# Kernel optimization log

Hardware: AMD Instinct MI355X
Metric: run time of the kernel (lower is better)

Reference implementation:

```python
import jax, jax.numpy as jnp
import numpy as np

N_NODES = 50000
N_EDGES = 800000
F_NODE = 128
F_EDGE = 32
H = 64


def _gat_layer(x, row, col, e_emb, W, le_W, att_src, att_dst, att_edge, bias):
    """PyG GATConv (heads=1, concat=True) with edge_dim, incl. self loops.
    x: [N, Fin]; row/col: [E] int (src, dst); e_emb: [E, H].
    """
    N = x.shape[0]
    loop = jnp.arange(N, dtype=row.dtype)
    row_a = jnp.concatenate([row, loop])
    col_a = jnp.concatenate([col, loop])
    # self-loop edge attr = mean of edge embeddings (PyG fill_value='mean')
    e_mean = jnp.mean(e_emb, axis=0)
    e_all = jnp.concatenate([e_emb, jnp.broadcast_to(e_mean, (N, e_emb.shape[1]))], axis=0)

    h = x @ W.T                      # [N, H]
    a_src = h @ att_src              # [N]
    a_dst = h @ att_dst              # [N]
    a_edge = (e_all @ le_W.T) @ att_edge  # [E+N]

    alpha = jax.nn.leaky_relu(a_src[row_a] + a_dst[col_a] + a_edge, negative_slope=0.2)
    # segment softmax over destination node neighborhoods
    m = jax.ops.segment_max(alpha, col_a, num_segments=N)
    ex = jnp.exp(alpha - m[col_a])
    denom = jax.ops.segment_sum(ex, col_a, num_segments=N)
    w = ex / denom[col_a]            # [E+N]
    out = jax.ops.segment_sum(h[row_a] * w[:, None], col_a, num_segments=N)
    return out + bias


def setup_inputs() -> dict:
    key = jax.random.key(0)
    ks = jax.random.split(key, 20)
    s = 0.1
    inp = {
        "x": jax.random.normal(ks[0], (N_NODES, F_NODE), dtype=jnp.float32),
        "edge_attr": jax.random.normal(ks[1], (N_EDGES, F_EDGE), dtype=jnp.float32),
        "edge_index": jax.random.randint(ks[2], (2, N_EDGES), 0, N_NODES, dtype=jnp.int32),
        # edge encoder (Linear with bias)
        "enc_W": jax.random.normal(ks[3], (H, F_EDGE), dtype=jnp.float32) * s,
        "enc_b": jnp.zeros((H,), dtype=jnp.float32),
        # conv1 params
        "W1": jax.random.normal(ks[4], (H, F_NODE), dtype=jnp.float32) * s,
        "le1_W": jax.random.normal(ks[5], (H, H), dtype=jnp.float32) * s,
        "as1": jax.random.normal(ks[6], (H,), dtype=jnp.float32) * s,
        "ad1": jax.random.normal(ks[7], (H,), dtype=jnp.float32) * s,
        "ae1": jax.random.normal(ks[8], (H,), dtype=jnp.float32) * s,
        "b1": jnp.zeros((H,), dtype=jnp.float32),
        # conv2 params
        "W2": jax.random.normal(ks[9], (H, H), dtype=jnp.float32) * s,
        "le2_W": jax.random.normal(ks[10], (H, H), dtype=jnp.float32) * s,
        "as2": jax.random.normal(ks[11], (H,), dtype=jnp.float32) * s,
        "ad2": jax.random.normal(ks[12], (H,), dtype=jnp.float32) * s,
        "ae2": jax.random.normal(ks[13], (H,), dtype=jnp.float32) * s,
        "b2": jnp.zeros((H,), dtype=jnp.float32),
        # edge scorer MLP: Linear(2H, H) -> ReLU -> Linear(H, 1)
        "s1_W": jax.random.normal(ks[14], (H, 2 * H), dtype=jnp.float32) * s,
        "s1_b": jnp.zeros((H,), dtype=jnp.float32),
        "s2_W": jax.random.normal(ks[15], (1, H), dtype=jnp.float32) * s,
        "s2_b": jnp.zeros((1,), dtype=jnp.float32),
    }
    return inp


def reference(x, edge_attr, edge_index, enc_W, enc_b,
              W1, le1_W, as1, ad1, ae1, b1,
              W2, le2_W, as2, ad2, ae2, b2,
              s1_W, s1_b, s2_W, s2_b):
    row, col = edge_index[0], edge_index[1]
    edge_emb = edge_attr @ enc_W.T + enc_b           # [E, H]
    h = jax.nn.relu(_gat_layer(x, row, col, edge_emb, W1, le1_W, as1, ad1, ae1, b1))
    # dropout p=0.5 is identity in eval mode
    h = _gat_layer(h, row, col, edge_emb, W2, le2_W, as2, ad2, ae2, b2)
    ef = jnp.concatenate([h[row], h[col]], axis=1)   # [E, 2H]
    z = jax.nn.relu(ef @ s1_W.T + s1_b) @ s2_W.T + s2_b  # [E, 1]
    return jax.nn.sigmoid(z).squeeze(-1)             # [E]
```

## Files before the change

kernel.cpp:

```cpp
#include <hip/hip_runtime.h>
#include <cstdint>
#include <cstddef>

#define NN 50000
#define NE 800000
#define FN 128
#define FE 32
#define HD 64
#define SCAN_NB ((NN + 255) / 256)
#define EP_NB (NE / 256)
#define GM_NB ((NN + 63) / 64)

__device__ __forceinline__ float lrelu(float x) { return x > 0.f ? x : 0.2f * x; }

__device__ __forceinline__ unsigned omap(float f) {
  unsigned u = __float_as_uint(f);
  return (u & 0x80000000u) ? ~u : (u | 0x80000000u);
}
__device__ __forceinline__ float odec(unsigned u) {
  return __uint_as_float((u & 0x80000000u) ? (u ^ 0x80000000u) : ~u);
}

__global__ void k_small0(const float* __restrict__ le1W, const float* __restrict__ ae1,
                         const float* __restrict__ le2W, const float* __restrict__ ae2,
                         const float* __restrict__ encW, const float* __restrict__ encb,
                         const float* __restrict__ s1W,
                         float* __restrict__ small, float* __restrict__ Scomb) {
  __shared__ float sv1[64], sv2[64];
  int t = threadIdx.x;
  float v1 = 0.f, v2 = 0.f;
  for (int j = 0; j < 64; ++j) {
    v1 += le1W[j * 64 + t] * ae1[j];
    v2 += le2W[j * 64 + t] * ae2[j];
  }
  sv1[t] = v1; sv2[t] = v2;
  small[t] = v1; small[64 + t] = v2;
  float cb1 = encb[t] * v1, cb2 = encb[t] * v2;
  #pragma unroll
  for (int m = 32; m; m >>= 1) { cb1 += __shfl_xor(cb1, m); cb2 += __shfl_xor(cb2, m); }
  __syncthreads();
  if (t < 32) {
    float p1 = 0.f, p2 = 0.f;
    for (int i = 0; i < 64; ++i) {
      p1 += encW[i * 32 + t] * sv1[i];
      p2 += encW[i * 32 + t] * sv2[i];
    }
    small[128 + t] = p1; small[160 + t] = p2;
  }
  if (t == 0) { small[192] = cb1; small[193] = cb2; }
  for (int j = 0; j < 64; ++j) {
    Scomb[j * 64 + t] = s1W[j * 128 + t];
    Scomb[(64 + j) * 64 + t] = s1W[j * 128 + 64 + t];
  }
}

__global__ __launch_bounds__(256) void k_scanA(const int* __restrict__ counts,
                                               int* __restrict__ loc, int* __restrict__ blocksums) {
  int tid = threadIdx.x;
  int i = blockIdx.x * 256 + tid;
  int v = (i < NN) ? counts[i] : 0;
  int lane = tid & 63, wid = tid >> 6;
  int x = v;
  #pragma unroll
  for (int d = 1; d < 64; d <<= 1) {
    int y = __shfl_up(x, d);
    if (lane >= d) x += y;
  }
  __shared__ int ws[4], wpref[4];
  if (lane == 63) ws[wid] = x;
  __syncthreads();
  if (tid == 0) {
    int run = 0;
    #pragma unroll
    for (int w = 0; w < 4; ++w) { wpref[w] = run; run += ws[w]; }
    blocksums[blockIdx.x] = run;
  }
  __syncthreads();
  if (i < NN) loc[i] = x - v + wpref[wid];
}

__global__ __launch_bounds__(256) void k_scanB(int* __restrict__ blocksums, int* __restrict__ offa,
                                               float* __restrict__ small) {
  int tid = threadIdx.x;
  int v = (tid < SCAN_NB) ? blocksums[tid] : 0;
  int lane = tid & 63, wid = tid >> 6;
  int x = v;
  #pragma unroll
  for (int d = 1; d < 64; d <<= 1) {
    int y = __shfl_up(x, d);
    if (lane >= d) x += y;
  }
  __shared__ int ws[4], wpref[4];
  if (lane == 63) ws[wid] = x;
  __syncthreads();
  if (tid == 0) {
    int run = 0;
    #pragma unroll
    for (int w = 0; w < 4; ++w) { wpref[w] = run; run += ws[w]; }
    offa[NN] = run;
    small[194] = small[228] * (1.0f / NE);
    small[195] = small[229] * (1.0f / NE);
  }
  __syncthreads();
  if (tid < SCAN_NB) blocksums[tid] = x - v + wpref[wid];
}

__global__ __launch_bounds__(256) void k_scanC(int* __restrict__ offa, const int* __restrict__ blocksums) {
  int i = blockIdx.x * 256 + threadIdx.x;
  if (i < NN) offa[i] = offa[i] + blocksums[blockIdx.x];
}

__global__ __launch_bounds__(256) void k_fused0(const float* __restrict__ attr,
                                                const int* __restrict__ col,
                                                const float* __restrict__ small,
                                                float* __restrict__ a_e1, float* __restrict__ a_e2,
                                                int* __restrict__ rank,
                                                int* __restrict__ counts,
                                                float* __restrict__ sums,
                                                unsigned* __restrict__ maxi,
                                                const float* __restrict__ x, const float* __restrict__ W1,
                                                float* __restrict__ h1,
                                                const float* __restrict__ as, const float* __restrict__ ad,
                                                float* __restrict__ asrc, float* __restrict__ adst) {
  __shared__ float smem[8704];
  int tid = threadIdx.x;
  if (blockIdx.x < EP_NB) {
    float* sattr = smem;
    float* redbuf = smem + 8448;
    float sp1[32], sp2[32];
    #pragma unroll
    for (int j = 0; j < 8; ++j) {
      float4 v1 = ((const float4*)(small + 128))[j];
      float4 v2 = ((const float4*)(small + 160))[j];
      sp1[j*4+0] = v1.x; sp1[j*4+1] = v1.y; sp1[j*4+2] = v1.z; sp1[j*4+3] = v1.w;
      sp2[j*4+0] = v2.x; sp2[j*4+1] = v2.y; sp2[j*4+2] = v2.z; sp2[j*4+3] = v2.w;
    }
    float c1 = small[192], c2 = small[193];
    int e = blockIdx.x * 256 + tid;
    int c = col[e];
    const float4* ain = (const float4*)(attr + (size_t)blockIdx.x * 256 * FE);
    #pragma unroll
    for (int it = 0; it < 8; ++it) {
      int idx = it * 256 + tid;
      float4 v = ain[idx];
      int r = idx >> 3, ch = idx & 7;
      float* dst = &sattr[r * 33 + ch * 4];
      dst[0] = v.x; dst[1] = v.y; dst[2] = v.z; dst[3] = v.w;
    }
    __syncthreads();
    const float* myrow = &sattr[tid * 33];
    float d1 = c1, d2 = c2;
    #pragma unroll
    for (int j = 0; j < 32; ++j) {
      float a = myrow[j];
      d1 += a * sp1[j];
      d2 += a * sp2[j];
    }
    a_e1[e] = d1;
    a_e2[e] = d2;
    rank[e] = atomicAdd(&counts[c], 1);
    float s1 = d1, s2 = d2, m1 = d1, m2 = d2;
    #pragma unroll
    for (int m = 32; m; m >>= 1) {
      s1 += __shfl_xor(s1, m); s2 += __shfl_xor(s2, m);
      m1 = fmaxf(m1, __shfl_xor(m1, m)); m2 = fmaxf(m2, __shfl_xor(m2, m));
    }
    int wid = tid >> 6;
    if ((tid & 63) == 0) { redbuf[wid] = s1; redbuf[4 + wid] = s2; redbuf[8 + wid] = m1; redbuf[12 + wid] = m2; }
    __syncthreads();
    if (tid == 0) atomicAdd(&sums[0], redbuf[0] + redbuf[1] + redbuf[2] + redbuf[3]);
    if (tid == 1) atomicAdd(&sums[1], redbuf[4] + redbuf[5] + redbuf[6] + redbuf[7]);
    if (tid == 2) atomicMax(&maxi[2], omap(fmaxf(fmaxf(redbuf[8], redbuf[9]), fmaxf(redbuf[10], redbuf[11]))));
    if (tid == 3) atomicMax(&maxi[3], omap(fmaxf(fmaxf(redbuf[12], redbuf[13]), fmaxf(redbuf[14], redbuf[15]))));
  } else {
    float (*At)[68] = (float(*)[68])smem;
    float (*Bt)[68] = (float(*)[68])(smem + 4352);
    int m0 = (blockIdx.x - EP_NB) * 64;
    float acc[4][4] = {};
    for (int kc = 0; kc < 128; kc += 64) {
      #pragma unroll
      for (int it = 0; it < 4; ++it) {
        int idx = it * 256 + tid;
        int m = idx & 63, kv = idx >> 6;
        float4 bv = ((const float4*)(W1 + (size_t)m * 128 + kc))[kv];
        Bt[kv*4+0][m] = bv.x; Bt[kv*4+1][m] = bv.y; Bt[kv*4+2][m] = bv.z; Bt[kv*4+3][m] = bv.w;
        int gm = m0 + m;
        float4 av = make_float4(0.f, 0.f, 0.f, 0.f);
        if (gm < NN) av = ((const float4*)(x + (size_t)gm * 128 + kc))[kv];
        At[kv*4+0][m] = av.x; At[kv*4+1][m] = av.y; At[kv*4+2][m] = av.z; At[kv*4+3][m] = av.w;
      }
      __syncthreads();
      int tn = tid & 15, tm = tid >> 4;
      #pragma unroll 8
      for (int k = 0; k < 64; ++k) {
        float4 a4 = *(const float4*)&At[k][tm * 4];
        float4 b4 = *(const float4*)&Bt[k][tn * 4];
        acc[0][0] += a4.x*b4.x; acc[0][1] += a4.x*b4.y; acc[0][2] += a4.x*b4.z; acc[0][3] += a4.x*b4.w;
        acc[1][0] += a4.y*b4.x; acc[1][1] += a4.y*b4.y; acc[1][2] += a4.y*b4.z; acc[1][3] += a4.y*b4.w;
        acc[2][0] += a4.z*b4.x; acc[2][1] += a4.z*b4.y; acc[2][2] += a4.z*b4.z; acc[2][3] += a4.z*b4.w;
        acc[3][0] += a4.w*b4.x; acc[3][1] += a4.w*b4.y; acc[3][2] += a4.w*b4.z; acc[3][3] += a4.w*b4.w;
      }
      __syncthreads();
    }
    int tn = tid & 15, tm = tid >> 4;
    #pragma unroll
    for (int i = 0; i < 4; ++i) {
      int gm = m0 + tm * 4 + i;
      if (gm < NN) {
        float4 o = make_float4(acc[i][0], acc[i][1], acc[i][2], acc[i][3]);
        *(float4*)(h1 + (size_t)gm * 64 + tn * 4) = o;
      }
    }
    __shared__ float wmax[4];
    float4 asv = ((const float4*)as)[tn];
    float4 adv = ((const float4*)ad)[tn];
    float smax = -1e30f;
    #pragma unroll
    for (int i = 0; i < 4; ++i) {
      float s = acc[i][0]*asv.x + acc[i][1]*asv.y + acc[i][2]*asv.z + acc[i][3]*asv.w;
      float d = acc[i][0]*adv.x + acc[i][1]*adv.y + acc[i][2]*adv.z + acc[i][3]*adv.w;
      #pragma unroll
      for (int m = 8; m; m >>= 1) { s += __shfl_xor(s, m, 16); d += __shfl_xor(d, m, 16); }
      int gm = m0 + tm * 4 + i;
      if (tn == 0 && gm < NN) { asrc[gm] = s; adst[gm] = d; smax = fmaxf(smax, s); }
    }
    #pragma unroll
    for (int m = 32; m; m >>= 1) smax = fmaxf(smax, __shfl_xor(smax, m));
    if ((tid & 63) == 0) wmax[tid >> 6] = smax;
    __syncthreads();
    if (tid == 0)
      atomicMax(&maxi[0], omap(fmaxf(fmaxf(wmax[0], wmax[1]), fmaxf(wmax[2], wmax[3]))));
  }
}

__global__ __launch_bounds__(256) void k_scatter(const int* __restrict__ row, const int* __restrict__ col,
                                                 const float* __restrict__ a_e1, const float* __restrict__ a_e2,
                                                 const int* __restrict__ rank, const int* __restrict__ offa,
                                                 int4* __restrict__ pk) {
  int t = blockIdx.x * 256 + threadIdx.x;
  if (t >= NE / 2) return;
  int e0 = t, e1 = t + NE / 2;
  int c0 = col[e0], c1 = col[e1];
  int r0 = rank[e0], r1 = rank[e1];
  int o0 = offa[c0], o1 = offa[c1];
  int4 q0, q1;
  q0.x = row[e0]; q0.y = __float_as_int(a_e1[e0]); q0.z = __float_as_int(a_e2[e0]); q0.w = 0;
  q1.x = row[e1]; q1.y = __float_as_int(a_e1[e1]); q1.z = __float_as_int(a_e2[e1]); q1.w = 0;
  pk[o0 + r0] = q0;
  pk[o1 + r1] = q1;
}

template <int K, int ASD>
__global__ __launch_bounds__(256) void k_gemm(const float* __restrict__ A, const float* __restrict__ B,
                                              float* __restrict__ C, int M, int ldc,
                                              const float* __restrict__ as, const float* __restrict__ ad,
                                              float* __restrict__ asrc, float* __restrict__ adst,
                                              unsigned* __restrict__ maxslot) {
  __shared__ float At[64][68];
  __shared__ float Bt[64][68];
  int tid = threadIdx.x;
  int m0 = blockIdx.x * 64;
  const float* Bp = B + (size_t)blockIdx.y * 64 * K;
  float acc[4][4] = {};
  for (int kc = 0; kc < K; kc += 64) {
    #pragma unroll
    for (int it = 0; it < 4; ++it) {
      int idx = it * 256 + tid;
      int m = idx & 63, kv = idx >> 6;
      float4 bv = ((const float4*)(Bp + (size_t)m * K + kc))[kv];
      Bt[kv*4+0][m] = bv.x; Bt[kv*4+1][m] = bv.y; Bt[kv*4+2][m] = bv.z; Bt[kv*4+3][m] = bv.w;
      int gm = m0 + m;
      float4 av = make_float4(0.f, 0.f, 0.f, 0.f);
      if (gm < M) av = ((const float4*)(A + (size_t)gm * K + kc))[kv];
      At[kv*4+0][m] = av.x; At[kv*4+1][m] = av.y; At[kv*4+2][m] = av.z; At[kv*4+3][m] = av.w;
    }
    __syncthreads();
    int tn = tid & 15, tm = tid >> 4;
    #pragma unroll 8
    for (int k = 0; k < 64; ++k) {
      float4 a4 = *(const float4*)&At[k][tm * 4];
      float4 b4 = *(const float4*)&Bt[k][tn * 4];
      acc[0][0] += a4.x*b4.x; acc[0][1] += a4.x*b4.y; acc[0][2] += a4.x*b4.z; acc[0][3] += a4.x*b4.w;
      acc[1][0] += a4.y*b4.x; acc[1][1] += a4.y*b4.y; acc[1][2] += a4.y*b4.z; acc[1][3] += a4.y*b4.w;
      acc[2][0] += a4.z*b4.x; acc[2][1] += a4.z*b4.y; acc[2][2] += a4.z*b4.z; acc[2][3] += a4.z*b4.w;
      acc[3][0] += a4.w*b4.x; acc[3][1] += a4.w*b4.y; acc[3][2] += a4.w*b4.z; acc[3][3] += a4.w*b4.w;
    }
    __syncthreads();
  }
  int tn = tid & 15, tm = tid >> 4;
  #pragma unroll
  for (int i = 0; i < 4; ++i) {
    int gm = m0 + tm * 4 + i;
    if (gm < M) {
      float4 o = make_float4(acc[i][0], acc[i][1], acc[i][2], acc[i][3]);
      *(float4*)(C + (size_t)gm * ldc + blockIdx.y * 64 + tn * 4) = o;
    }
  }
  if constexpr (ASD) {
    __shared__ float wmax[4];
    float4 asv = ((const float4*)as)[tn];
    float4 adv = ((const float4*)ad)[tn];
    float smax = -1e30f;
    #pragma unroll
    for (int i = 0; i < 4; ++i) {
      float s = acc[i][0]*asv.x + acc[i][1]*asv.y + acc[i][2]*asv.z + acc[i][3]*asv.w;
      float d = acc[i][0]*adv.x + acc[i][1]*adv.y + acc[i][2]*adv.z + acc[i][3]*adv.w;
      #pragma unroll
      for (int m = 8; m; m >>= 1) { s += __shfl_xor(s, m, 16); d += __shfl_xor(d, m, 16); }
      int gm = m0 + tm * 4 + i;
      if (tn == 0 && gm < M) { asrc[gm] = s; adst[gm] = d; smax = fmaxf(smax, s); }
    }
    #pragma unroll
    for (int m = 32; m; m >>= 1) smax = fmaxf(smax, __shfl_xor(smax, m));
    if ((tid & 63) == 0) wmax[tid >> 6] = smax;
    __syncthreads();
    if (tid == 0)
      atomicMax(maxslot, omap(fmaxf(fmaxf(wmax[0], wmax[1]), fmaxf(wmax[2], wmax[3]))));
  }
}

__global__ __launch_bounds__(256) void k_agg(const float* __restrict__ h, const int* __restrict__ offa,
                                             const int4* __restrict__ pk, int comp,
                                             const float* __restrict__ asrc, const float* __restrict__ adst,
                                             const float* __restrict__ small, int selfIdx,
                                             const unsigned* __restrict__ maxi,
                                             const float* __restrict__ bias, float* __restrict__ outp,
                                             int do_relu) {
  int gt = blockIdx.x * 256 + threadIdx.x;
  int n = gt >> 6, lane = gt & 63;
  if (n >= NN) return;
  int beg = offa[n], end = offa[n + 1];
  float adn = adst[n];
  float mx = lrelu(odec(maxi[comp]) + adn + odec(maxi[2 + comp]));
  float alpha_self = lrelu(asrc[n] + adn + small[selfIdx]);
  float ex_self = __expf(alpha_self - mx);
  float denom = ex_self;
  float acc0 = ex_self * h[(size_t)n * 64 + lane];
  float acc1 = 0.f, acc2 = 0.f, acc3 = 0.f;
  for (int base = beg; base < end; base += 64) {
    int p = base + lane;
    int cnt = min(64, end - base);
    float ex = 0.f; int s = 0;
    if (p < end) {
      int4 q = pk[p];
      s = q.x;
      float ae = __int_as_float(comp ? q.z : q.y);
      ex = __expf(lrelu(asrc[s] + adn + ae) - mx);
    }
    float exs = ex;
    #pragma unroll
    for (int m = 32; m; m >>= 1) exs += __shfl_xor(exs, m);
    denom += exs;
    int q4 = cnt & ~3;
    for (int q = 0; q < q4; q += 4) {
      float e0 = __shfl(ex, q),     e1 = __shfl(ex, q + 1);
      float e2 = __shfl(ex, q + 2), e3 = __shfl(ex, q + 3);
      int s0 = __shfl(s, q),     s1 = __shfl(s, q + 1);
      int s2 = __shfl(s, q + 2), s3 = __shfl(s, q + 3);
      acc0 += e0 * h[(size_t)s0 * 64 + lane];
      acc1 += e1 * h[(size_t)s1 * 64 + lane];
      acc2 += e2 * h[(size_t)s2 * 64 + lane];
      acc3 += e3 * h[(size_t)s3 * 64 + lane];
    }
    for (int q = q4; q < cnt; ++q) {
      float eq = __shfl(ex, q);
      int sq = __shfl(s, q);
      acc0 += eq * h[(size_t)sq * 64 + lane];
    }
  }
  float r = (acc0 + acc1 + acc2 + acc3) / denom + bias[lane];
  if (do_relu) r = fmaxf(r, 0.f);
  outp[(size_t)n * 64 + lane] = r;
}

__global__ __launch_bounds__(256) void k_final(const int* __restrict__ row, const int* __restrict__ col,
                                               const float* __restrict__ uv, const float* __restrict__ s1b,
                                               const float* __restrict__ s2w, const float* __restrict__ s2b,
                                               float* __restrict__ outp) {
  int gt = blockIdx.x * 256 + threadIdx.x;
  int e = gt >> 4, i = gt & 15;
  if (e >= NE) return;
  int r = row[e], c = col[e];
  float4 a = ((const float4*)(uv + (size_t)r * 128))[i];
  float4 b = ((const float4*)(uv + (size_t)c * 128 + 64))[i];
  float4 bb = ((const float4*)s1b)[i];
  float4 ww = ((const float4*)s2w)[i];
  float z = fmaxf(a.x + b.x + bb.x, 0.f) * ww.x
          + fmaxf(a.y + b.y + bb.y, 0.f) * ww.y
          + fmaxf(a.z + b.z + bb.z, 0.f) * ww.z
          + fmaxf(a.w + b.w + bb.w, 0.f) * ww.w;
  #pragma unroll
  for (int m = 1; m < 16; m <<= 1) z += __shfl_xor(z, m, 16);
  if (i == 0) outp[e] = 1.f / (1.f + __expf(-(z + s2b[0])));
}

extern "C" void kernel_launch(void* const* d_in, const int* in_sizes, int n_in,
                              void* d_out, int out_size, void* d_ws, size_t ws_size,
                              hipStream_t stream) {
  const float* x    = (const float*)d_in[0];
  const float* attr = (const float*)d_in[1];
  const int*   eidx = (const int*)d_in[2];
  const float* encW = (const float*)d_in[3];
  const float* encb = (const float*)d_in[4];
  const float* W1   = (const float*)d_in[5];
  const float* le1W = (const float*)d_in[6];
  const float* as1  = (const float*)d_in[7];
  const float* ad1  = (const float*)d_in[8];
  const float* ae1w = (const float*)d_in[9];
  const float* b1   = (const float*)d_in[10];
  const float* W2   = (const float*)d_in[11];
  const float* le2W = (const float*)d_in[12];
  const float* as2  = (const float*)d_in[13];
  const float* ad2  = (const float*)d_in[14];
  const float* ae2w = (const float*)d_in[15];
  const float* b2   = (const float*)d_in[16];
  const float* s1W  = (const float*)d_in[17];
  const float* s1b  = (const float*)d_in[18];
  const float* s2w  = (const float*)d_in[19];
  const float* s2b  = (const float*)d_in[20];
  float* outp = (float*)d_out;

  const int* row = eidx;
  const int* col = eidx + NE;

  char* p = (char*)d_ws;
  auto alloc = [&](size_t bytes) { char* r = p; p += (bytes + 255) & ~(size_t)255; return r; };
  float* small = (float*)alloc(1024);
  unsigned* maxi = (unsigned*)alloc(256);
  float* Scomb = (float*)alloc(8192 * 4);
  int*   counts= (int*)alloc((size_t)NN * 4);
  int*   offa  = (int*)alloc((size_t)(NN + 1) * 4);
  int*   bsums = (int*)alloc((size_t)SCAN_NB * 4);
  float* a_e1  = (float*)alloc((size_t)NE * 4);
  float* a_e2  = (float*)alloc((size_t)NE * 4);
  int*   rank  = (int*)alloc((size_t)NE * 4);
  int4*  pk    = (int4*)alloc((size_t)NE * 16);
  float* h1    = (float*)alloc((size_t)NN * 64 * 4);
  float* out1  = (float*)alloc((size_t)NN * 64 * 4);
  float* h2    = (float*)alloc((size_t)NN * 64 * 4);
  float* out2  = (float*)alloc((size_t)NN * 64 * 4);
  float* asrc1 = (float*)alloc((size_t)NN * 4);
  float* adst1 = (float*)alloc((size_t)NN * 4);
  float* asrc2 = (float*)alloc((size_t)NN * 4);
  float* adst2 = (float*)alloc((size_t)NN * 4);
  float* uv = h1;

  hipMemsetAsync(small, 0, 1024, stream);
  hipMemsetAsync(maxi, 0, 256, stream);
  hipMemsetAsync(counts, 0, (size_t)NN * 4, stream);

  k_small0<<<1, 64, 0, stream>>>(le1W, ae1w, le2W, ae2w, encW, encb, s1W, small, Scomb);
  k_fused0<<<EP_NB + GM_NB, 256, 0, stream>>>(attr, col, small, a_e1, a_e2, rank, counts,
                                              small + 228, maxi, x, W1, h1, as1, ad1, asrc1, adst1);
  k_scanA<<<SCAN_NB, 256, 0, stream>>>(counts, offa, bsums);
  k_scanB<<<1, 256, 0, stream>>>(bsums, offa, small);
  k_scanC<<<SCAN_NB, 256, 0, stream>>>(offa, bsums);
  k_scatter<<<(NE / 2 + 255) / 256, 256, 0, stream>>>(row, col, a_e1, a_e2, rank, offa, pk);

  k_agg<<<(NN * 64) / 256, 256, 0, stream>>>(h1, offa, pk, 0, asrc1, adst1,
                                             small, 194, maxi, b1, out1, 1);
  k_gemm<64, 1><<<dim3((NN + 63) / 64, 1), 256, 0, stream>>>(out1, W2, h2, NN, 64, as2, ad2, asrc2, adst2, maxi + 1);
  k_agg<<<(NN * 64) / 256, 256, 0, stream>>>(h2, offa, pk, 1, asrc2, adst2,
                                             small, 195, maxi, b2, out2, 0);
  k_gemm<64, 0><<<dim3((NN + 63) / 64, 2), 256, 0, stream>>>(out2, Scomb, uv, NN, 128, nullptr, nullptr, nullptr, nullptr, nullptr);
  k_final<<<(NE * 16) / 256, 256, 0, stream>>>(row, col, uv, s1b, s2w, s2b, outp);
}
```

Baseline: 318.7 us.

## Iterate edge scorer over destination-sorted CSR to reuse destination features

The final edge-scoring kernel now runs one wavefront per destination node over the CSR-sorted packed edge list instead of one 16-lane group per original edge. The destination half of uv plus the bias is loaded once per node, and the original edge id is stored in the packed record so outputs are written back to their original positions. This removes the per-edge col lookup and the destination gather, but it brings scattered output writes and load imbalance across nodes with different degrees.

```diff
diff --git a/kernel.cpp b/kernel.cpp
--- a/kernel.cpp
+++ b/kernel.cpp
@@ -244,8 +244,8 @@
   int r0 = rank[e0], r1 = rank[e1];
   int o0 = offa[c0], o1 = offa[c1];
   int4 q0, q1;
-  q0.x = row[e0]; q0.y = __float_as_int(a_e1[e0]); q0.z = __float_as_int(a_e2[e0]); q0.w = 0;
-  q1.x = row[e1]; q1.y = __float_as_int(a_e1[e1]); q1.z = __float_as_int(a_e2[e1]); q1.w = 0;
+  q0.x = row[e0]; q0.y = __float_as_int(a_e1[e0]); q0.z = __float_as_int(a_e2[e0]); q0.w = e0;
+  q1.x = row[e1]; q1.y = __float_as_int(a_e1[e1]); q1.z = __float_as_int(a_e2[e1]); q1.w = e1;
   pk[o0 + r0] = q0;
   pk[o1 + r1] = q1;
 }
@@ -373,25 +373,46 @@
   outp[(size_t)n * 64 + lane] = r;
 }
 
-__global__ __launch_bounds__(256) void k_final(const int* __restrict__ row, const int* __restrict__ col,
+__global__ __launch_bounds__(256) void k_final(const int* __restrict__ offa, const int4* __restrict__ pk,
                                                const float* __restrict__ uv, const float* __restrict__ s1b,
                                                const float* __restrict__ s2w, const float* __restrict__ s2b,
                                                float* __restrict__ outp) {
   int gt = blockIdx.x * 256 + threadIdx.x;
-  int e = gt >> 4, i = gt & 15;
-  if (e >= NE) return;
-  int r = row[e], c = col[e];
-  float4 a = ((const float4*)(uv + (size_t)r * 128))[i];
-  float4 b = ((const float4*)(uv + (size_t)c * 128 + 64))[i];
+  int n = gt >> 6, lane = gt & 63;
+  if (n >= NN) return;
+  int g = lane >> 4, i = lane & 15;
+  int beg = offa[n], end = offa[n + 1];
+  float4 v4 = ((const float4*)(uv + (size_t)n * 128 + 64))[i];
   float4 bb = ((const float4*)s1b)[i];
   float4 ww = ((const float4*)s2w)[i];
-  float z = fmaxf(a.x + b.x + bb.x, 0.f) * ww.x
-          + fmaxf(a.y + b.y + bb.y, 0.f) * ww.y
-          + fmaxf(a.z + b.z + bb.z, 0.f) * ww.z
-          + fmaxf(a.w + b.w + bb.w, 0.f) * ww.w;
-  #pragma unroll
-  for (int m = 1; m < 16; m <<= 1) z += __shfl_xor(z, m, 16);
-  if (i == 0) outp[e] = 1.f / (1.f + __expf(-(z + s2b[0])));
+  float4 vb = make_float4(v4.x + bb.x, v4.y + bb.y, v4.z + bb.z, v4.w + bb.w);
+  float sb = s2b[0];
+  int p = beg + g;
+  for (; p + 4 < end; p += 8) {
+    int4 qa = pk[p];
+    int4 qb = pk[p + 4];
+    float4 ua = ((const float4*)(uv + (size_t)qa.x * 128))[i];
+    float4 ub = ((const float4*)(uv + (size_t)qb.x * 128))[i];
+    float za = fmaxf(ua.x + vb.x, 0.f) * ww.x + fmaxf(ua.y + vb.y, 0.f) * ww.y
+             + fmaxf(ua.z + vb.z, 0.f) * ww.z + fmaxf(ua.w + vb.w, 0.f) * ww.w;
+    float zb = fmaxf(ub.x + vb.x, 0.f) * ww.x + fmaxf(ub.y + vb.y, 0.f) * ww.y
+             + fmaxf(ub.z + vb.z, 0.f) * ww.z + fmaxf(ub.w + vb.w, 0.f) * ww.w;
+    #pragma unroll
+    for (int m = 1; m < 16; m <<= 1) { za += __shfl_xor(za, m, 16); zb += __shfl_xor(zb, m, 16); }
+    if (i == 0) {
+      outp[qa.w] = 1.f / (1.f + __expf(-(za + sb)));
+      outp[qb.w] = 1.f / (1.f + __expf(-(zb + sb)));
+    }
+  }
+  if (p < end) {
+    int4 q = pk[p];
+    float4 u = ((const float4*)(uv + (size_t)q.x * 128))[i];
+    float z = fmaxf(u.x + vb.x, 0.f) * ww.x + fmaxf(u.y + vb.y, 0.f) * ww.y
+            + fmaxf(u.z + vb.z, 0.f) * ww.z + fmaxf(u.w + vb.w, 0.f) * ww.w;
+    #pragma unroll
+    for (int m = 1; m < 16; m <<= 1) z += __shfl_xor(z, m, 16);
+    if (i == 0) outp[q.w] = 1.f / (1.f + __expf(-(z + sb)));
+  }
 }
 
 extern "C" void kernel_launch(void* const* d_in, const int* in_sizes, int n_in,
@@ -463,5 +484,5 @@
   k_agg<<<(NN * 64) / 256, 256, 0, stream>>>(h2, offa, pk, 1, asrc2, adst2,
                                              small, 195, maxi, b2, out2, 0);
   k_gemm<64, 0><<<dim3((NN + 63) / 64, 2), 256, 0, stream>>>(out2, Scomb, uv, NN, 128, nullptr, nullptr, nullptr, nullptr, nullptr);
-  k_final<<<(NE * 16) / 256, 256, 0, stream>>>(row, col, uv, s1b, s2w, s2b, outp);
-}
+  k_final<<<(NN * 64) / 256, 256, 0, stream>>>(offa, pk, uv, s1b, s2w, s2b, outp);
+}
```

After: 304.0 us. -4.6%, faster.
